# Kernel tuning notes

Hardware: AMD Instinct MI355X
Metric: run time of the kernel (lower is better)

Reference implementation:

```python
import jax, jax.numpy as jnp
import numpy as np

N_NODES = 100000

def _sage_conv(x, edge_index, w_l, b_l, w_r):
    # PyG SAGEConv (mean aggr): out = lin_l(mean_j x_j) + lin_r(x)
    src, dst = edge_index[0], edge_index[1]
    msgs = x[src]  # [E, F] gather
    agg = jax.ops.segment_sum(msgs, dst, num_segments=N_NODES)
    cnt = jax.ops.segment_sum(jnp.ones((edge_index.shape[1],), x.dtype), dst, num_segments=N_NODES)
    agg = agg / jnp.maximum(cnt, 1.0)[:, None]  # mean; isolated nodes -> 0
    return agg @ w_l.T + b_l + x @ w_r.T

def setup_inputs() -> dict:
    key = jax.random.key(0)
    k = jax.random.split(key, 8)
    in_c, hid, out_c = 128, 64, 32
    x = jax.random.normal(k[0], (N_NODES, in_c), dtype=jnp.float32)
    edge_index = jax.random.randint(k[1], (2, 600000), 0, N_NODES, dtype=jnp.int64)
    s = lambda kk, fo, fi: jax.random.normal(kk, (fo, fi), jnp.float32) / jnp.sqrt(fi)
    return {
        'x': x,
        'edge_index': edge_index,
        'w1_l': s(k[2], hid, in_c),
        'b1_l': jnp.zeros((hid,), jnp.float32),
        'w1_r': s(k[3], hid, in_c),
        'w2_l': s(k[4], out_c, hid),
        'b2_l': jnp.zeros((out_c,), jnp.float32),
        'w2_r': s(k[5], out_c, hid),
    }

def reference(x, edge_index, w1_l, b1_l, w1_r, w2_l, b2_l, w2_r):
    h = _sage_conv(x, edge_index, w1_l, b1_l, w1_r)
    h = jax.nn.relu(h)
    # dropout(p=0.3) is identity in eval mode
    return _sage_conv(h, edge_index, w2_l, b2_l, w2_r)
```

## Files before the change

kernel.cpp:

```cpp
#include <hip/hip_runtime.h>

#define N_NODES 100000
#define N_EDGES 600000
#define N_PAD   100352
#define CAP     40
#define G1_TILES 3125
#define G1_TPB   4
#define G1_BLOCKS 782
#define CSR_EPB 2048
#define CSR_BLOCKS 293
#define FRONT_BLOCKS 1078
#define MID_BLOCKS 3125

typedef __bf16 bf16x8 __attribute__((ext_vector_type(8)));
typedef float  f32x4  __attribute__((ext_vector_type(4)));
typedef unsigned short u16x8 __attribute__((ext_vector_type(8)));
typedef unsigned short u16x4 __attribute__((ext_vector_type(4)));

__device__ inline unsigned short f2bf(float f) {
    __bf16 h = (__bf16)f;
    return __builtin_bit_cast(unsigned short, h);
}
__device__ inline float bf2f(unsigned short u) {
    return __builtin_bit_cast(float, ((unsigned)u) << 16);
}
__device__ inline bf16x8 ldfrag_bf16(const unsigned short* p) {
    u16x8 v = *(const u16x8*)p;
    return __builtin_bit_cast(bf16x8, v);
}

__global__ __launch_bounds__(256) void prep(
    const float* __restrict__ w1l, const float* __restrict__ w1r,
    const float* __restrict__ w2l, const float* __restrict__ w2r,
    unsigned short* __restrict__ wbf1, unsigned short* __restrict__ wbf2,
    int* __restrict__ deg)
{
    int i = blockIdx.x * 256 + threadIdx.x;
    deg[i] = 0;
    if (i < 16384) {
        int row = i >> 7, k = i & 127;
        float v = (row < 64) ? w1l[(row << 7) + k] : w1r[((row - 64) << 7) + k];
        wbf1[i] = f2bf(v);
    } else if (i < 20480) {
        int j = i - 16384;
        int row = j >> 6, k = j & 63;
        float v = (row < 32) ? w2l[(row << 6) + k] : w2r[((row - 32) << 6) + k];
        wbf2[j] = f2bf(v);
    }
}

__global__ __launch_bounds__(256) void front(
    const float* __restrict__ x,
    const unsigned short* __restrict__ wbf1,
    const int* __restrict__ ei,
    unsigned short* __restrict__ xl,
    unsigned short* __restrict__ xr,
    int* __restrict__ deg,
    int* __restrict__ csr32)
{
    const int b   = blockIdx.x;
    const int tid = threadIdx.x;
    const int grp = b / 11;
    const int r   = b - grp * 11;

    if (r >= 8) {
        const int cb = grp * 3 + (r - 8);
        if (cb >= CSR_BLOCKS) return;
        const int e0 = cb * CSR_EPB + tid;
        #pragma unroll
        for (int rr = 0; rr < 8; ++rr) {
            int e = e0 + rr * 256;
            if (e < N_EDGES) {
                int d = ei[N_EDGES + e];
                int pos = atomicAdd(&deg[d], 1);
                if (pos < CAP) csr32[d * CAP + pos] = ei[e];
            }
        }
        return;
    }

    const int gb = grp * 8 + r;
    if (gb >= G1_BLOCKS) return;

    __shared__ unsigned short wlds[128 * 128];
    __shared__ unsigned short xs[2][32 * 128];

    #pragma unroll
    for (int i = 0; i < 8; ++i) {
        int idx = i * 256 + tid;
        int row = idx >> 4;
        int off = (idx & 15) << 4;
        u16x8 v = *(const u16x8*)(wbf1 + row * 128 + (off >> 1));
        *(u16x8*)((char*)wlds + row * 256 + (off ^ ((row & 7) << 4))) = v;
    }

    const int t0     = gb * G1_TPB;
    const int ntiles = (G1_TILES - t0 < G1_TPB) ? (G1_TILES - t0) : G1_TPB;

    const int wv   = tid >> 6;
    const int l    = tid & 63;
    const int lrow = l & 15;
    const int hi   = l >> 4;
    const int sr0  = tid >> 4;
    const int soff = (tid & 15) << 4;

    float4 pf[4];

    #define SLOAD(t) do {                                                      \
        _Pragma("unroll")                                                      \
        for (int rr = 0; rr < 2; ++rr) {                                       \
            const float* src = x + (size_t)((t) * 32 + sr0 + rr * 16) * 128    \
                                 + (soff >> 1);                                \
            pf[2*rr]   = *(const float4*)src;                                  \
            pf[2*rr+1] = *(const float4*)(src + 4);                            \
        }                                                                      \
    } while (0)

    #define SWRITE(bf) do {                                                    \
        _Pragma("unroll")                                                      \
        for (int rr = 0; rr < 2; ++rr) {                                       \
            int row = sr0 + rr * 16;                                           \
            u16x8 o;                                                           \
            o[0]=f2bf(pf[2*rr].x);   o[1]=f2bf(pf[2*rr].y);                    \
            o[2]=f2bf(pf[2*rr].z);   o[3]=f2bf(pf[2*rr].w);                    \
            o[4]=f2bf(pf[2*rr+1].x); o[5]=f2bf(pf[2*rr+1].y);                  \
            o[6]=f2bf(pf[2*rr+1].z); o[7]=f2bf(pf[2*rr+1].w);                  \
            *(u16x8*)((char*)&xs[bf][0] + row * 256                            \
                      + (soff ^ ((row & 7) << 4))) = o;                        \
        }                                                                      \
    } while (0)

    SLOAD(t0);
    SWRITE(0);
    __syncthreads();

    for (int tt = 0; tt < ntiles; ++tt) {
        if (tt + 1 < ntiles) SLOAD(t0 + tt + 1);

        char* xb = (char*)&xs[tt & 1][0];
        f32x4 acc[2][2];
        #pragma unroll
        for (int nt = 0; nt < 2; ++nt)
            #pragma unroll
            for (int ft = 0; ft < 2; ++ft) acc[nt][ft] = (f32x4){0.f,0.f,0.f,0.f};

        #pragma unroll
        for (int kt = 0; kt < 4; ++kt) {
            const int koff = kt * 64 + hi * 16;
            const int r0 = lrow, r1 = 16 + lrow;
            bf16x8 b0 = __builtin_bit_cast(bf16x8, *(const u16x8*)
                (xb + r0 * 256 + (koff ^ ((r0 & 7) << 4))));
            bf16x8 b1 = __builtin_bit_cast(bf16x8, *(const u16x8*)
                (xb + r1 * 256 + (koff ^ ((r1 & 7) << 4))));
            #pragma unroll
            for (int ft = 0; ft < 2; ++ft) {
                const int fr = wv * 32 + ft * 16 + lrow;
                bf16x8 a = __builtin_bit_cast(bf16x8, *(const u16x8*)
                    ((char*)wlds + fr * 256 + (koff ^ ((fr & 7) << 4))));
                acc[0][ft] = __builtin_amdgcn_mfma_f32_16x16x32_bf16(a, b0, acc[0][ft], 0, 0, 0);
                acc[1][ft] = __builtin_amdgcn_mfma_f32_16x16x32_bf16(a, b1, acc[1][ft], 0, 0, 0);
            }
        }

        if (tt + 1 < ntiles) SWRITE((tt + 1) & 1);
        __syncthreads();

        #pragma unroll
        for (int nt = 0; nt < 2; ++nt) {
            const int node = nt * 16 + lrow;
            #pragma unroll
            for (int ft = 0; ft < 2; ++ft) {
                const int fb = (wv * 32 + ft * 16 + hi * 4) * 2;
                u16x4 p;
                p[0] = f2bf(acc[nt][ft][0]); p[1] = f2bf(acc[nt][ft][1]);
                p[2] = f2bf(acc[nt][ft][2]); p[3] = f2bf(acc[nt][ft][3]);
                *(u16x4*)(xb + node * 256 + (fb ^ ((node & 7) << 4))) = p;
            }
        }
        __syncthreads();

        const int nbase = (t0 + tt) * 32;
        #pragma unroll
        for (int rr = 0; rr < 2; ++rr) {
            int idx = rr * 256 + tid;
            int row = idx >> 4;
            int off = (idx & 15) << 4;
            u16x8 v = *(const u16x8*)(xb + row * 256 + (off ^ ((row & 7) << 4)));
            if (off < 128) *(u16x8*)&xl[(nbase + row) * 64 + (off >> 1)] = v;
            else           *(u16x8*)&xr[(nbase + row) * 64 + ((off - 128) >> 1)] = v;
        }
        __syncthreads();
    }
    #undef SLOAD
    #undef SWRITE
}

__global__ __launch_bounds__(256) void mid(
    const unsigned short* __restrict__ xl,
    const unsigned short* __restrict__ xr,
    const int* __restrict__ deg,
    const int* __restrict__ csr32,
    const float* __restrict__ b1l,
    const unsigned short* __restrict__ wbf2,
    unsigned short* __restrict__ hl,
    unsigned short* __restrict__ hr)
{
    __shared__ unsigned short hs[32 * 64];

    const int tid = threadIdx.x;
    const int nd  = tid >> 3;
    const int q   = tid & 7;
    const int node = blockIdx.x * 32 + nd;

    const int beg = node * CAP;
    const int dg  = min(deg[node], CAP);

    float acc[8] = {0.f,0.f,0.f,0.f,0.f,0.f,0.f,0.f};
    int i = 0;
    for (; i + 4 <= dg; i += 4) {
        int s0 = csr32[beg + i];
        int s1 = csr32[beg + i + 1];
        int s2 = csr32[beg + i + 2];
        int s3 = csr32[beg + i + 3];
        u16x8 v0 = *(const u16x8*)&xl[s0 * 64 + 8 * q];
        u16x8 v1 = *(const u16x8*)&xl[s1 * 64 + 8 * q];
        u16x8 v2 = *(const u16x8*)&xl[s2 * 64 + 8 * q];
        u16x8 v3 = *(const u16x8*)&xl[s3 * 64 + 8 * q];
        #pragma unroll
        for (int j = 0; j < 8; ++j)
            acc[j] += (bf2f(v0[j]) + bf2f(v1[j])) + (bf2f(v2[j]) + bf2f(v3[j]));
    }
    for (; i < dg; ++i) {
        int s = csr32[beg + i];
        u16x8 v = *(const u16x8*)&xl[s * 64 + 8 * q];
        #pragma unroll
        for (int j = 0; j < 8; ++j) acc[j] += bf2f(v[j]);
    }
    const float inv = 1.0f / (float)max(dg, 1);
    u16x8 rv = *(const u16x8*)&xr[node * 64 + 8 * q];
    float4 b0 = *(const float4*)&b1l[8 * q];
    float4 b1 = *(const float4*)&b1l[8 * q + 4];
    float bb[8] = {b0.x,b0.y,b0.z,b0.w,b1.x,b1.y,b1.z,b1.w};
    u16x8 hv;
    #pragma unroll
    for (int j = 0; j < 8; ++j) {
        float o = fmaf(acc[j], inv, bb[j]) + bf2f(rv[j]);
        hv[j] = f2bf(fmaxf(o, 0.f));
    }
    *(u16x8*)((char*)hs + nd * 128 + ((q * 16) ^ ((nd & 7) << 4))) = hv;
    __syncthreads();

    const int wv   = tid >> 6;
    const int l    = tid & 63;
    const int lrow = l & 15;
    const int hi   = l >> 4;

    f32x4 a0 = (f32x4){0.f,0.f,0.f,0.f};
    f32x4 a1 = (f32x4){0.f,0.f,0.f,0.f};
    #pragma unroll
    for (int kt = 0; kt < 2; ++kt) {
        const int kin = kt * 64 + hi * 16;
        bf16x8 bf0 = __builtin_bit_cast(bf16x8, *(const u16x8*)
            ((const char*)hs + lrow * 128 + (kin ^ ((lrow & 7) << 4))));
        bf16x8 bf1 = __builtin_bit_cast(bf16x8, *(const u16x8*)
            ((const char*)hs + (16 + lrow) * 128 + (kin ^ ((lrow & 7) << 4))));
        bf16x8 a = ldfrag_bf16(wbf2 + (wv * 16 + lrow) * 64 + kt * 32 + hi * 8);
        a0 = __builtin_amdgcn_mfma_f32_16x16x32_bf16(a, bf0, a0, 0, 0, 0);
        a1 = __builtin_amdgcn_mfma_f32_16x16x32_bf16(a, bf1, a1, 0, 0, 0);
    }
    __syncthreads();

    {
        const int c2 = (wv * 16 + hi * 4) * 2;
        u16x4 p0, p1;
        p0[0]=f2bf(a0[0]); p0[1]=f2bf(a0[1]); p0[2]=f2bf(a0[2]); p0[3]=f2bf(a0[3]);
        p1[0]=f2bf(a1[0]); p1[1]=f2bf(a1[1]); p1[2]=f2bf(a1[2]); p1[3]=f2bf(a1[3]);
        const int n0l = lrow, n1l = 16 + lrow;
        *(u16x4*)((char*)hs + n0l * 128 + (c2 ^ ((n0l & 7) << 4))) = p0;
        *(u16x4*)((char*)hs + n1l * 128 + (c2 ^ ((n1l & 7) << 4))) = p1;
    }
    __syncthreads();

    {
        const int row = tid >> 3;
        const int off = (tid & 7) << 4;
        u16x8 v = *(const u16x8*)((char*)hs + row * 128 + (off ^ ((row & 7) << 4)));
        const int gn = blockIdx.x * 32 + row;
        if (off < 64) *(u16x8*)&hl[gn * 32 + (off >> 1)] = v;
        else          *(u16x8*)&hr[gn * 32 + ((off - 64) >> 1)] = v;
    }
}

__global__ __launch_bounds__(256) void gather2(
    const unsigned short* __restrict__ hl,
    const int* __restrict__ deg,
    const int* __restrict__ csr32,
    const float* __restrict__ b2l,
    const unsigned short* __restrict__ hr,
    float* __restrict__ out)
{
    int t = blockIdx.x * 256 + threadIdx.x;
    int n = t >> 2;
    int q = t & 3;
    if (n >= N_NODES) return;
    int beg = n * CAP, dg = min(deg[n], CAP);

    float acc[8] = {0.f,0.f,0.f,0.f,0.f,0.f,0.f,0.f};
    int i = 0;
    for (; i + 4 <= dg; i += 4) {
        int s0 = csr32[beg + i];
        int s1 = csr32[beg + i + 1];
        int s2 = csr32[beg + i + 2];
        int s3 = csr32[beg + i + 3];
        u16x8 v0 = *(const u16x8*)&hl[s0 * 32 + 8 * q];
        u16x8 v1 = *(const u16x8*)&hl[s1 * 32 + 8 * q];
        u16x8 v2 = *(const u16x8*)&hl[s2 * 32 + 8 * q];
        u16x8 v3 = *(const u16x8*)&hl[s3 * 32 + 8 * q];
        #pragma unroll
        for (int j = 0; j < 8; ++j)
            acc[j] += (bf2f(v0[j]) + bf2f(v1[j])) + (bf2f(v2[j]) + bf2f(v3[j]));
    }
    for (; i < dg; ++i) {
        int s = csr32[beg + i];
        u16x8 v = *(const u16x8*)&hl[s * 32 + 8 * q];
        #pragma unroll
        for (int j = 0; j < 8; ++j) acc[j] += bf2f(v[j]);
    }
    float inv = 1.0f / (float)max(dg, 1);
    u16x8 rv = *(const u16x8*)&hr[n * 32 + 8 * q];
    float4 b0 = *(const float4*)&b2l[8 * q];
    float4 b1 = *(const float4*)&b2l[8 * q + 4];
    float bb[8] = {b0.x,b0.y,b0.z,b0.w,b1.x,b1.y,b1.z,b1.w};
    float o[8];
    #pragma unroll
    for (int j = 0; j < 8; ++j)
        o[j] = fmaf(acc[j], inv, bb[j]) + bf2f(rv[j]);
    float* op = out + n * 32 + 8 * q;
    *(float4*)op       = make_float4(o[0], o[1], o[2], o[3]);
    *(float4*)(op + 4) = make_float4(o[4], o[5], o[6], o[7]);
}

extern "C" void kernel_launch(void* const* d_in, const int* in_sizes, int n_in,
                              void* d_out, int out_size, void* d_ws, size_t ws_size,
                              hipStream_t stream)
{
    const float* x   = (const float*)d_in[0];
    const int*   ei  = (const int*)d_in[1];
    const float* w1l = (const float*)d_in[2];
    const float* b1l = (const float*)d_in[3];
    const float* w1r = (const float*)d_in[4];
    const float* w2l = (const float*)d_in[5];
    const float* b2l = (const float*)d_in[6];
    const float* w2r = (const float*)d_in[7];
    float* out = (float*)d_out;

    char* ws = (char*)d_ws;
    unsigned short* xl   = (unsigned short*)(ws + 0);
    unsigned short* xr   = (unsigned short*)(ws + 12800000);
    unsigned short* hl   = (unsigned short*)(ws + 25600000);
    unsigned short* hr   = (unsigned short*)(ws + 32000000);
    int* csr32 = (int*)(ws + 38400000);
    int* deg   = (int*)(ws + 54400000);
    unsigned short* wbf1 = (unsigned short*)(ws + 54801408);
    unsigned short* wbf2 = (unsigned short*)(ws + 54834176);

    prep<<<392, 256, 0, stream>>>(w1l, w1r, w2l, w2r, wbf1, wbf2, deg);
    front<<<FRONT_BLOCKS, 256, 0, stream>>>(x, wbf1, ei, xl, xr, deg, csr32);
    mid<<<MID_BLOCKS, 256, 0, stream>>>(xl, xr, deg, csr32, b1l, wbf2, hl, hr);
    gather2<<<(N_NODES * 4 + 255) / 256, 256, 0, stream>>>(hl, deg, csr32, b2l, hr, out);
}
```

Measured before the change: 84.76 us.

## Rebalance front kernel: 5 tiles per GEMM block, batched CSR loads, contiguous block split

The GEMM part of the front kernel now gives each block 5 tiles, which divides the 3125 tiles evenly, so the tail bounds check is dropped and the tile loop has a fixed count. CSR-build blocks now handle 17 edges per thread and load all src/dst indices before issuing the atomics, which exposes more memory parallelism and cuts the CSR block count. The interleaved 8:3 block mapping is replaced by a contiguous split, GEMM blocks first and CSR blocks after. The larger per-thread arrays may raise register use, and CSR blocks may now start only after the GEMM blocks are dispatched.

```diff
diff --git a/kernel.cpp b/kernel.cpp
--- a/kernel.cpp
+++ b/kernel.cpp
@@ -5,11 +5,12 @@
 #define N_PAD   100352
 #define CAP     40
 #define G1_TILES 3125
-#define G1_TPB   4
-#define G1_BLOCKS 782
-#define CSR_EPB 2048
-#define CSR_BLOCKS 293
-#define FRONT_BLOCKS 1078
+#define G1_TPB   5
+#define G1_BLOCKS 625
+#define CSR_EPT 17
+#define CSR_EPB (CSR_EPT * 256)
+#define CSR_BLOCKS 138
+#define FRONT_BLOCKS (G1_BLOCKS + CSR_BLOCKS)
 #define MID_BLOCKS 3125
 
 typedef __bf16 bf16x8 __attribute__((ext_vector_type(8)));
@@ -60,27 +61,26 @@
 {
     const int b   = blockIdx.x;
     const int tid = threadIdx.x;
-    const int grp = b / 11;
-    const int r   = b - grp * 11;
-
-    if (r >= 8) {
-        const int cb = grp * 3 + (r - 8);
-        if (cb >= CSR_BLOCKS) return;
+
+    if (b >= G1_BLOCKS) {
+        const int cb = b - G1_BLOCKS;
         const int e0 = cb * CSR_EPB + tid;
-        #pragma unroll
-        for (int rr = 0; rr < 8; ++rr) {
+        int dst[CSR_EPT], src[CSR_EPT];
+        #pragma unroll
+        for (int rr = 0; rr < CSR_EPT; ++rr) {
             int e = e0 + rr * 256;
-            if (e < N_EDGES) {
-                int d = ei[N_EDGES + e];
-                int pos = atomicAdd(&deg[d], 1);
-                if (pos < CAP) csr32[d * CAP + pos] = ei[e];
+            if (e < N_EDGES) { dst[rr] = ei[N_EDGES + e]; src[rr] = ei[e]; }
+            else             { dst[rr] = -1; }
+        }
+        #pragma unroll
+        for (int rr = 0; rr < CSR_EPT; ++rr) {
+            if (dst[rr] >= 0) {
+                int pos = atomicAdd(&deg[dst[rr]], 1);
+                if (pos < CAP) csr32[dst[rr] * CAP + pos] = src[rr];
             }
         }
         return;
     }
-
-    const int gb = grp * 8 + r;
-    if (gb >= G1_BLOCKS) return;
 
     __shared__ unsigned short wlds[128 * 128];
     __shared__ unsigned short xs[2][32 * 128];
@@ -94,8 +94,7 @@
         *(u16x8*)((char*)wlds + row * 256 + (off ^ ((row & 7) << 4))) = v;
     }
 
-    const int t0     = gb * G1_TPB;
-    const int ntiles = (G1_TILES - t0 < G1_TPB) ? (G1_TILES - t0) : G1_TPB;
+    const int t0 = b * G1_TPB;
 
     const int wv   = tid >> 6;
     const int l    = tid & 63;
@@ -134,8 +133,8 @@
     SWRITE(0);
     __syncthreads();
 
-    for (int tt = 0; tt < ntiles; ++tt) {
-        if (tt + 1 < ntiles) SLOAD(t0 + tt + 1);
+    for (int tt = 0; tt < G1_TPB; ++tt) {
+        if (tt + 1 < G1_TPB) SLOAD(t0 + tt + 1);
 
         char* xb = (char*)&xs[tt & 1][0];
         f32x4 acc[2][2];
@@ -162,7 +161,7 @@
             }
         }
 
-        if (tt + 1 < ntiles) SWRITE((tt + 1) & 1);
+        if (tt + 1 < G1_TPB) SWRITE((tt + 1) & 1);
         __syncthreads();
 
         #pragma unroll
```

Result: faster. 78.42 us (-7.5%).
